# Optimization experiments

Measured on AMD Instinct MI355X. Metric: run time of the kernel, lower is better.

## Reference

```python
import jax, jax.numpy as jnp
import numpy as np

B, N, DIM = 8, 1024, 768
HEADS, HEAD_DIM = 12, 64
INNER = HEADS * HEAD_DIM  # 768
SCALE = HEAD_DIM ** -0.5


def setup_inputs() -> dict:
    key = jax.random.key(0)
    k1, k2, k3, k4 = jax.random.split(key, 4)
    x = jax.random.normal(k1, (B, N, DIM), dtype=jnp.float32)
    # nn.Linear weights, stored as (in, out) for x @ W
    w_qkv = jax.random.normal(k2, (DIM, 3 * INNER), dtype=jnp.float32) * (DIM ** -0.5)
    w_out = jax.random.normal(k3, (INNER, DIM), dtype=jnp.float32) * (INNER ** -0.5)
    b_out = jax.random.normal(k4, (DIM,), dtype=jnp.float32) * 0.02
    return {"x": x, "w_qkv": w_qkv, "w_out": w_out, "b_out": b_out}


def reference(x, w_qkv, w_out, b_out):
    qkv = jnp.einsum('bnd,de->bne', x, w_qkv)  # [B, N, 3*INNER]
    q, k, v = jnp.split(qkv, 3, axis=-1)
    # 'b n (h d) -> b h n d'
    def split_heads(t):
        return t.reshape(B, N, HEADS, HEAD_DIM).transpose(0, 2, 1, 3)
    q, k, v = split_heads(q), split_heads(k), split_heads(v)
    score = jnp.einsum('bhnd,bhmd->bhnm', q, k) * SCALE  # [B, H, N, N]
    # Faithful to torch nn.Softmax() with dim=None on a 4D tensor: legacy
    # behavior applies softmax over dim=1 (the HEADS axis), NOT the key axis.
    attention = jax.nn.softmax(score, axis=1)
    out = jnp.einsum('bhnm,bhmd->bhnd', attention, v)  # [B, H, N, D]
    out = out.transpose(0, 2, 1, 3).reshape(B, N, INNER)  # 'b h n d -> b n (h d)'
    return jnp.einsum('bne,ed->bnd', out, w_out) + b_out
```

## Files before the change

### kernel.cpp

```cpp
#include <hip/hip_runtime.h>

typedef float  f32x4  __attribute__((ext_vector_type(4)));
typedef short  bf16x8 __attribute__((ext_vector_type(8)));

#define MFMA16(a, b, c) __builtin_amdgcn_mfma_f32_16x16x32_bf16((a), (b), (c), 0, 0, 0)

#define GLL16(g, l) __builtin_amdgcn_global_load_lds(                      \
    (const __attribute__((address_space(1))) void*)(g),                    \
    (__attribute__((address_space(3))) void*)(l), 16, 0, 0)

__device__ __forceinline__ short f2bf(float f) {
    union { float f; unsigned u; } a; a.f = f;
    unsigned r = a.u + 0x7fffu + ((a.u >> 16) & 1u);
    return (short)(r >> 16);
}
__device__ __forceinline__ float bf2f(unsigned short u) {
    union { unsigned u; float f; } a; a.u = ((unsigned)u) << 16; return a.f;
}

#define Bb   8
#define Nn   1024
#define DIM  768
#define HH   12
#define HD   64
#define INNER 768
#define SCALE 0.125f
#define SCL2E 0.18033688011112042f

__global__ void cast_to_bf16(const float* __restrict__ in, short* __restrict__ out, int n4) {
    int i = blockIdx.x * 256 + threadIdx.x;
    if (i >= n4) return;
    float4 f = reinterpret_cast<const float4*>(in)[i];
    unsigned lo = (unsigned)(unsigned short)f2bf(f.x) | ((unsigned)(unsigned short)f2bf(f.y) << 16);
    unsigned hi = (unsigned)(unsigned short)f2bf(f.z) | ((unsigned)(unsigned short)f2bf(f.w) << 16);
    reinterpret_cast<uint2*>(out)[i] = make_uint2(lo, hi);
}

__global__ void transpose_cast(const float* __restrict__ w, short* __restrict__ wt,
                               int rows, int cols) {
    int idx = blockIdx.x * 256 + threadIdx.x;
    if (idx >= rows * cols) return;
    int c = idx / rows;
    int k = idx - c * rows;
    wt[idx] = f2bf(w[k * cols + c]);
}

template <int MODE>
__global__ __launch_bounds__(256, 4)
void gemm128(const short* __restrict__ A, const short* __restrict__ Bt, int K,
             short* __restrict__ qb, short* __restrict__ kb, short* __restrict__ vtb,
             float* __restrict__ outp, const float* __restrict__ bias) {
    __shared__ __align__(16) short As[2][128 * 32];
    __shared__ __align__(16) short Bs[2][128 * 32];

    const int tid  = threadIdx.x;
    const int lane = tid & 63, wv = tid >> 6;
    const int wrow = wv >> 1, wcol = wv & 1;
    const int quad = lane >> 4, l16 = lane & 15;
    const int m0 = blockIdx.y * 128, n0 = blockIdx.x * 128;

    const int row64 = (wv << 4) + (lane >> 2);
    const int gu = (lane & 3) ^ ((lane >> 3) & 3);
    const size_t aoff = (size_t)(m0 + row64) * K + gu * 8;
    const size_t boff = (size_t)(n0 + row64) * K + gu * 8;
    const int lch = wv * 512;

    f32x4 acc[4][4];
#pragma unroll
    for (int i = 0; i < 4; i++)
#pragma unroll
        for (int j = 0; j < 4; j++) acc[i][j] = (f32x4){0.f, 0.f, 0.f, 0.f};

    GLL16(A  + aoff,                   &As[0][lch]);
    GLL16(A  + aoff + (size_t)64 * K,  &As[0][2048 + lch]);
    GLL16(Bt + boff,                   &Bs[0][lch]);
    GLL16(Bt + boff + (size_t)64 * K,  &Bs[0][2048 + lch]);

    const int swo = (quad ^ ((l16 >> 1) & 3)) * 8;

    const int NK = K >> 5;
    for (int ks = 0; ks < NK; ks++) {
        asm volatile("s_waitcnt vmcnt(0)" ::: "memory");
        __syncthreads();
        if (ks + 1 < NK) {
            const int pn = (ks + 1) & 1;
            const int kc = (ks + 1) << 5;
            GLL16(A  + aoff + kc,                  &As[pn][lch]);
            GLL16(A  + aoff + (size_t)64 * K + kc, &As[pn][2048 + lch]);
            GLL16(Bt + boff + kc,                  &Bs[pn][lch]);
            GLL16(Bt + boff + (size_t)64 * K + kc, &Bs[pn][2048 + lch]);
        }
        const int pb = ks & 1;

        bf16x8 af[4], bfr[4];
#pragma unroll
        for (int t = 0; t < 4; t++)
            af[t] = *reinterpret_cast<bf16x8*>(&As[pb][(wrow * 64 + t * 16 + l16) * 32 + swo]);
#pragma unroll
        for (int t = 0; t < 4; t++)
            bfr[t] = *reinterpret_cast<bf16x8*>(&Bs[pb][(wcol * 64 + t * 16 + l16) * 32 + swo]);
#pragma unroll
        for (int rt = 0; rt < 4; rt++)
#pragma unroll
            for (int ct = 0; ct < 4; ct++)
                acc[rt][ct] = MFMA16(af[rt], bfr[ct], acc[rt][ct]);
    }

#pragma unroll
    for (int rt = 0; rt < 4; rt++) {
#pragma unroll
        for (int ct = 0; ct < 4; ct++) {
            const int c = n0 + wcol * 64 + ct * 16 + l16;
#pragma unroll
            for (int reg = 0; reg < 4; reg++) {
                const int r = m0 + wrow * 64 + rt * 16 + quad * 4 + reg;
                const float v = acc[rt][ct][reg];
                if (MODE == 0) {
                    const int b = r >> 10, n = r & 1023;
                    const int which = (c >= 1536) ? 2 : (c >= 768 ? 1 : 0);
                    const int cc = c - which * 768;
                    const int h = cc >> 6, d = cc & 63;
                    const int bh = b * HH + h;
                    const short bv = f2bf(v);
                    if (which == 0)      qb[(bh << 16) + (n << 6) + d] = bv;
                    else if (which == 1) kb[(bh << 16) + (n << 6) + d] = bv;
                    else                 vtb[(bh << 16) + (d << 10) + n] = bv;
                } else {
                    outp[(size_t)r * 768 + c] = v + bias[c];
                }
            }
        }
    }
}

__global__ __launch_bounds__(512, 4)
void attn_den5(const short* __restrict__ qb, const short* __restrict__ kb,
               short* __restrict__ invp) {
    __shared__ __align__(16) short Qs[2][128 * 64];
    __shared__ __align__(16) short Ks[2][128 * 64];

    const int tid = threadIdx.x, lane = tid & 63, wv = tid >> 6;
    const int wrow = wv >> 2, wcol = wv & 3;
    const int quad = lane >> 4, l16 = lane & 15;
    const int bid = blockIdx.x;
    const int b = bid & 7;
    const int nmt = bid >> 3;
    const int n0 = (nmt >> 3) << 7;
    const int m0 = (nmt & 7) << 7;

    const int r8 = lane >> 3;
    const int gu = (lane & 7) ^ r8;
    const int qo0 = (n0 + wv * 8 + r8) * 64 + gu * 8;
    const int qo1 = qo0 + 64 * 64;
    const int ko0 = (m0 + wv * 8 + r8) * 64 + gu * 8;
    const int ko1 = ko0 + 64 * 64;
    const int lc0 = wv * 512;
    const int lc1 = 4096 + wv * 512;

    f32x4 den[4][2];
#pragma unroll
    for (int i = 0; i < 4; i++)
#pragma unroll
        for (int j = 0; j < 2; j++) den[i][j] = (f32x4){0.f, 0.f, 0.f, 0.f};
    const f32x4 z = (f32x4){0.f, 0.f, 0.f, 0.f};

    {
        const short* qh = qb + ((size_t)(b * HH) << 16);
        const short* kh = kb + ((size_t)(b * HH) << 16);
        GLL16(qh + qo0, &Qs[0][lc0]);
        GLL16(qh + qo1, &Qs[0][lc1]);
        GLL16(kh + ko0, &Ks[0][lc0]);
        GLL16(kh + ko1, &Ks[0][lc1]);
    }

    for (int h = 0; h < HH; h++) {
        asm volatile("s_waitcnt vmcnt(0)" ::: "memory");
        __syncthreads();
        if (h < HH - 1) {
            const int pn = (h + 1) & 1;
            const short* qh = qb + ((size_t)(b * HH + h + 1) << 16);
            const short* kh = kb + ((size_t)(b * HH + h + 1) << 16);
            GLL16(qh + qo0, &Qs[pn][lc0]);
            GLL16(qh + qo1, &Qs[pn][lc1]);
            GLL16(kh + ko0, &Ks[pn][lc0]);
            GLL16(kh + ko1, &Ks[pn][lc1]);
        }
        const int pb = h & 1;
        const int sw0 = (quad ^ (l16 & 7)) * 8;

        bf16x8 aq[4][2], bk[2][2];
#pragma unroll
        for (int t = 0; t < 4; t++) {
            const int row = wrow * 64 + t * 16 + l16;
            aq[t][0] = *reinterpret_cast<bf16x8*>(&Qs[pb][row * 64 + sw0]);
            aq[t][1] = *reinterpret_cast<bf16x8*>(&Qs[pb][row * 64 + (sw0 ^ 32)]);
        }
#pragma unroll
        for (int t = 0; t < 2; t++) {
            const int row = wcol * 32 + t * 16 + l16;
            bk[t][0] = *reinterpret_cast<bf16x8*>(&Ks[pb][row * 64 + sw0]);
            bk[t][1] = *reinterpret_cast<bf16x8*>(&Ks[pb][row * 64 + (sw0 ^ 32)]);
        }
#pragma unroll
        for (int nt = 0; nt < 4; nt++)
#pragma unroll
            for (int mt = 0; mt < 2; mt++) {
                f32x4 s = MFMA16(aq[nt][0], bk[mt][0], z);
                s = MFMA16(aq[nt][1], bk[mt][1], s);
#pragma unroll
                for (int r = 0; r < 4; r++)
                    den[nt][mt][r] += __builtin_amdgcn_exp2f(s[r] * SCL2E);
            }
    }

#pragma unroll
    for (int nt = 0; nt < 4; nt++)
#pragma unroll
        for (int mt = 0; mt < 2; mt++) {
            const int ntg = (n0 >> 4) + wrow * 4 + nt;
            const int mtg = (m0 >> 4) + wcol * 2 + mt;
            ushort4 o;
            o.x = (unsigned short)f2bf(1.0f / den[nt][mt][0]);
            o.y = (unsigned short)f2bf(1.0f / den[nt][mt][1]);
            o.z = (unsigned short)f2bf(1.0f / den[nt][mt][2]);
            o.w = (unsigned short)f2bf(1.0f / den[nt][mt][3]);
            *reinterpret_cast<ushort4*>(&invp[(((b * 64 + ntg) * 64 + mtg) * 64 + lane) * 4]) = o;
        }
}

__global__ __launch_bounds__(256, 4)
void attn_pv2(const short* __restrict__ qb, const short* __restrict__ kb,
              const short* __restrict__ vtb, const short* __restrict__ invp,
              short* __restrict__ attn_out) {
    __shared__ __align__(16) short Ks[2][32 * 72];
    __shared__ __align__(16) short Vs[2][64 * 40];
    __shared__ __align__(16) short Ps[4][32 * 40];

    const int tid = threadIdx.x, lane = tid & 63, wv = tid >> 6;
    const int quad = lane >> 4, l16 = lane & 15;
    const int bid = blockIdx.x;
    const int b = bid & 7;
    const int r = bid >> 3;
    const int n4 = r / 12;
    const int h = r - n4 * 12;
    const int nb = n4 << 7;
    const int bh = b * HH + h;

    bf16x8 aq[2][2];
#pragma unroll
    for (int nt = 0; nt < 2; nt++) {
        const short* qp = qb + (bh << 16) + ((nb + wv * 32 + nt * 16 + l16) << 6) + quad * 8;
        aq[nt][0] = *reinterpret_cast<const bf16x8*>(qp);
        aq[nt][1] = *reinterpret_cast<const bf16x8*>(qp + 32);
    }

    const f32x4 z = (f32x4){0.f, 0.f, 0.f, 0.f};
    f32x4 O[2][4];
#pragma unroll
    for (int nt = 0; nt < 2; nt++)
#pragma unroll
        for (int d = 0; d < 4; d++) O[nt][d] = z;

    const int krow = tid >> 3, koff = (tid & 7) * 8;
    const int vrow = tid >> 2, voff = (tid & 3) * 8;

    uint4 kreg = *reinterpret_cast<const uint4*>(kb + (bh << 16) + (krow << 6) + koff);
    uint4 vreg = *reinterpret_cast<const uint4*>(vtb + (bh << 16) + (vrow << 10) + voff);

    for (int it = 0; it < 32; it++) {
        const int p = it & 1;
        *reinterpret_cast<uint4*>(&Ks[p][krow * 72 + koff]) = kreg;
        *reinterpret_cast<uint4*>(&Vs[p][vrow * 40 + voff]) = vreg;
        __syncthreads();
        if (it < 31) {
            const int m1 = (it + 1) << 5;
            kreg = *reinterpret_cast<const uint4*>(kb + (bh << 16) + ((m1 + krow) << 6) + koff);
            vreg = *reinterpret_cast<const uint4*>(vtb + (bh << 16) + (vrow << 10) + m1 + voff);
        }
        const int m0 = it << 5;

#pragma unroll
        for (int mh = 0; mh < 2; mh++) {
            const bf16x8 k0 = *reinterpret_cast<bf16x8*>(&Ks[p][(mh * 16 + l16) * 72 + quad * 8]);
            const bf16x8 k1 = *reinterpret_cast<bf16x8*>(&Ks[p][(mh * 16 + l16) * 72 + quad * 8 + 32]);
            const int mt = (m0 >> 4) + mh;
#pragma unroll
            for (int nt = 0; nt < 2; nt++) {
                f32x4 s = MFMA16(aq[nt][0], k0, z);
                s = MFMA16(aq[nt][1], k1, s);
                const int ntg = (nb >> 4) + wv * 2 + nt;
                const ushort4 iv = *reinterpret_cast<const ushort4*>(
                    &invp[(((b * 64 + ntg) * 64 + mt) * 64 + lane) * 4]);
                Ps[wv][(nt * 16 + quad * 4 + 0) * 40 + mh * 16 + l16] = f2bf(__expf(s[0] * SCALE) * bf2f(iv.x));
                Ps[wv][(nt * 16 + quad * 4 + 1) * 40 + mh * 16 + l16] = f2bf(__expf(s[1] * SCALE) * bf2f(iv.y));
                Ps[wv][(nt * 16 + quad * 4 + 2) * 40 + mh * 16 + l16] = f2bf(__expf(s[2] * SCALE) * bf2f(iv.z));
                Ps[wv][(nt * 16 + quad * 4 + 3) * 40 + mh * 16 + l16] = f2bf(__expf(s[3] * SCALE) * bf2f(iv.w));
            }
        }
        __threadfence_block();

        bf16x8 pa[2];
#pragma unroll
        for (int nt = 0; nt < 2; nt++)
            pa[nt] = *reinterpret_cast<bf16x8*>(&Ps[wv][(nt * 16 + l16) * 40 + quad * 8]);
#pragma unroll
        for (int dch = 0; dch < 4; dch++) {
            const bf16x8 vf = *reinterpret_cast<bf16x8*>(&Vs[p][(dch * 16 + l16) * 40 + quad * 8]);
#pragma unroll
            for (int nt = 0; nt < 2; nt++)
                O[nt][dch] = MFMA16(pa[nt], vf, O[nt][dch]);
        }
    }

#pragma unroll
    for (int nt = 0; nt < 2; nt++)
#pragma unroll
        for (int dch = 0; dch < 4; dch++) {
            const int col = h * 64 + dch * 16 + l16;
#pragma unroll
            for (int reg = 0; reg < 4; reg++) {
                const int n = nb + wv * 32 + nt * 16 + quad * 4 + reg;
                attn_out[(size_t)((b << 10) + n) * 768 + col] = f2bf(O[nt][dch][reg]);
            }
        }
}

extern "C" void kernel_launch(void* const* d_in, const int* in_sizes, int n_in,
                              void* d_out, int out_size, void* d_ws, size_t ws_size,
                              hipStream_t stream) {
    const float* x     = (const float*)d_in[0];
    const float* w_qkv = (const float*)d_in[1];
    const float* w_out = (const float*)d_in[2];
    const float* b_out = (const float*)d_in[3];
    float* out = (float*)d_out;

    short* xb   = (short*)d_ws;
    short* wT1  = xb  + 8192 * 768;
    short* wT2  = wT1 + 2304 * 768;
    short* qb   = wT2 + 768 * 768;
    short* kb   = qb  + 96 * 65536;
    short* vtb  = kb  + 96 * 65536;
    short* attn = vtb + 96 * 65536;
    short* invp = attn + 8192 * 768;

    cast_to_bf16<<<6144, 256, 0, stream>>>(x, xb, (8192 * 768) / 4);
    transpose_cast<<<(2304 * 768) / 256, 256, 0, stream>>>(w_qkv, wT1, 768, 2304);
    transpose_cast<<<(768 * 768) / 256, 256, 0, stream>>>(w_out, wT2, 768, 768);

    gemm128<0><<<dim3(2304 / 128, 8192 / 128), 256, 0, stream>>>(
        xb, wT1, 768, qb, kb, vtb, nullptr, nullptr);

    attn_den5<<<512, 512, 0, stream>>>(qb, kb, invp);
    attn_pv2<<<768, 256, 0, stream>>>(qb, kb, vtb, invp, attn);

    gemm128<1><<<dim3(768 / 128, 8192 / 128), 256, 0, stream>>>(
        attn, wT2, 768, nullptr, nullptr, nullptr, out, b_out);
}
```

Measured before the change: 257.4 us.

## Triple-buffer GEMM LDS tiles with prefetch distance two and split barriers

Moves the bf16 GEMM main loop from double buffering to a three-stage LDS ring. Global-to-LDS loads are issued two k-steps ahead, and the wait uses a partial vmcnt instead of draining every outstanding load. Each step reads its fragments from LDS before the barrier and raises wave priority around the MFMA block. The extra LDS buffer lowers the launch bound from 4 to 3 blocks per SM, which trades occupancy for a deeper memory pipeline.

```diff
diff --git a/kernel.cpp b/kernel.cpp
--- a/kernel.cpp
+++ b/kernel.cpp
@@ -45,13 +45,42 @@
     wt[idx] = f2bf(w[k * cols + c]);
 }
 
+#define STAGE(ksv, bv)                                                      \
+  { const int kc_ = (ksv) << 5;                                             \
+    GLL16(A  + aoff + kc_,                  &As[bv][lch]);                  \
+    GLL16(A  + aoff + (size_t)64 * K + kc_, &As[bv][2048 + lch]);           \
+    GLL16(Bt + boff + kc_,                  &Bs[bv][lch]);                  \
+    GLL16(Bt + boff + (size_t)64 * K + kc_, &Bs[bv][2048 + lch]); }
+
+#define PHASE(VM, DO_STAGE)                                                 \
+  {                                                                         \
+    bf16x8 af[4], bfr[4];                                                   \
+    _Pragma("unroll") for (int t = 0; t < 4; t++)                           \
+      af[t] = *reinterpret_cast<const bf16x8*>(                             \
+          &As[bi][(wrow * 64 + t * 16 + l16) * 32 + swo]);                  \
+    _Pragma("unroll") for (int t = 0; t < 4; t++)                           \
+      bfr[t] = *reinterpret_cast<const bf16x8*>(                            \
+          &Bs[bi][(wcol * 64 + t * 16 + l16) * 32 + swo]);                  \
+    if (DO_STAGE) { STAGE(ks + 2, bn); }                                    \
+    asm volatile("s_waitcnt vmcnt(" #VM ")" ::: "memory");                  \
+    __builtin_amdgcn_s_barrier();                                           \
+    asm volatile("s_waitcnt lgkmcnt(0)" ::: "memory");                      \
+    __builtin_amdgcn_sched_barrier(0);                                      \
+    __builtin_amdgcn_s_setprio(1);                                          \
+    _Pragma("unroll") for (int rt = 0; rt < 4; rt++)                        \
+      _Pragma("unroll") for (int ct = 0; ct < 4; ct++)                      \
+        acc[rt][ct] = MFMA16(af[rt], bfr[ct], acc[rt][ct]);                 \
+    __builtin_amdgcn_s_setprio(0);                                          \
+    __builtin_amdgcn_s_barrier();                                           \
+  }
+
 template <int MODE>
-__global__ __launch_bounds__(256, 4)
+__global__ __launch_bounds__(256, 3)
 void gemm128(const short* __restrict__ A, const short* __restrict__ Bt, int K,
              short* __restrict__ qb, short* __restrict__ kb, short* __restrict__ vtb,
              float* __restrict__ outp, const float* __restrict__ bias) {
-    __shared__ __align__(16) short As[2][128 * 32];
-    __shared__ __align__(16) short Bs[2][128 * 32];
+    __shared__ __align__(16) short As[3][128 * 32];
+    __shared__ __align__(16) short Bs[3][128 * 32];
 
     const int tid  = threadIdx.x;
     const int lane = tid & 63, wv = tid >> 6;
@@ -71,40 +100,25 @@
 #pragma unroll
         for (int j = 0; j < 4; j++) acc[i][j] = (f32x4){0.f, 0.f, 0.f, 0.f};
 
-    GLL16(A  + aoff,                   &As[0][lch]);
-    GLL16(A  + aoff + (size_t)64 * K,  &As[0][2048 + lch]);
-    GLL16(Bt + boff,                   &Bs[0][lch]);
-    GLL16(Bt + boff + (size_t)64 * K,  &Bs[0][2048 + lch]);
-
     const int swo = (quad ^ ((l16 >> 1) & 3)) * 8;
 
     const int NK = K >> 5;
-    for (int ks = 0; ks < NK; ks++) {
-        asm volatile("s_waitcnt vmcnt(0)" ::: "memory");
-        __syncthreads();
-        if (ks + 1 < NK) {
-            const int pn = (ks + 1) & 1;
-            const int kc = (ks + 1) << 5;
-            GLL16(A  + aoff + kc,                  &As[pn][lch]);
-            GLL16(A  + aoff + (size_t)64 * K + kc, &As[pn][2048 + lch]);
-            GLL16(Bt + boff + kc,                  &Bs[pn][lch]);
-            GLL16(Bt + boff + (size_t)64 * K + kc, &Bs[pn][2048 + lch]);
-        }
-        const int pb = ks & 1;
-
-        bf16x8 af[4], bfr[4];
-#pragma unroll
-        for (int t = 0; t < 4; t++)
-            af[t] = *reinterpret_cast<bf16x8*>(&As[pb][(wrow * 64 + t * 16 + l16) * 32 + swo]);
-#pragma unroll
-        for (int t = 0; t < 4; t++)
-            bfr[t] = *reinterpret_cast<bf16x8*>(&Bs[pb][(wcol * 64 + t * 16 + l16) * 32 + swo]);
-#pragma unroll
-        for (int rt = 0; rt < 4; rt++)
-#pragma unroll
-            for (int ct = 0; ct < 4; ct++)
-                acc[rt][ct] = MFMA16(af[rt], bfr[ct], acc[rt][ct]);
-    }
+
+    STAGE(0, 0);
+    STAGE(1, 1);
+    asm volatile("s_waitcnt vmcnt(4)" ::: "memory");
+    __builtin_amdgcn_s_barrier();
+
+    int bi = 0, bn = 2;
+    int ks = 0;
+    for (; ks < NK - 2; ks++) {
+        PHASE(4, true);
+        bi = (bi == 2) ? 0 : bi + 1;
+        bn = (bn == 2) ? 0 : bn + 1;
+    }
+    PHASE(0, false);
+    bi = (bi == 2) ? 0 : bi + 1;
+    PHASE(0, false);
 
 #pragma unroll
     for (int rt = 0; rt < 4; rt++) {
```

Result: no change. 256.0 us (-0.5%).
